# Optimization experiments

Measured on AMD Instinct MI355X. Metric: run time of the kernel, lower is better.

The kernel has to match this reference:

```python
import jax, jax.numpy as jnp
import numpy as np

NUM_HEADS = 16
D_MODEL = 1024
HEAD_DIM = D_MODEL // NUM_HEADS
NEG_BIG = 1e10


def setup_inputs() -> dict:
    key = jax.random.key(0)
    k1, k2, k3 = jax.random.split(key, 3)
    B, T = 2, 2048
    from_tensor = jax.random.normal(k1, (B, T, D_MODEL), dtype=jnp.float32)
    init = 0.02
    Wqkv = jax.random.normal(k2, (D_MODEL, 3 * D_MODEL), dtype=jnp.float32) * init
    bqkv = jnp.zeros((3 * D_MODEL,), dtype=jnp.float32)
    Wproj = jax.random.normal(k3, (D_MODEL, D_MODEL), dtype=jnp.float32) * init
    bproj = jnp.zeros((D_MODEL,), dtype=jnp.float32)
    return {"from_tensor": from_tensor, "Wqkv": Wqkv, "bqkv": bqkv,
            "Wproj": Wproj, "bproj": bproj}


def reference(from_tensor, Wqkv, bqkv, Wproj, bproj):
    B, T, D = from_tensor.shape
    H, hd = NUM_HEADS, D // NUM_HEADS
    qkv = from_tensor @ Wqkv + bqkv                      # [B,T,3D]
    q, k, v = jnp.split(qkv, 3, axis=-1)
    def heads(x):  # [B,T,D] -> [B,H,T,hd]
        return x.reshape(B, T, H, hd).transpose(0, 2, 1, 3)
    q, k, v = heads(q), heads(k), heads(v)
    present = jnp.stack([k, v], axis=1)                  # [B,2,H,T,hd]
    scores = jnp.einsum('bhqd,bhkd->bhqk', q, k)         # [B,H,T,T]
    scores = scores * jax.lax.rsqrt(jnp.float32(hd))
    # faithful mask: m = i > j - ns + nd (strict; diagonal masked)
    nd = ns = T
    i = jnp.arange(nd)[:, None]
    j = jnp.arange(ns)
    m = (i > j - ns + nd).astype(scores.dtype)           # [T,T]
    scores = scores * m - NEG_BIG * (1.0 - m)
    probs = jax.nn.softmax(scores, axis=-1)
    ctx = jnp.einsum('bhqk,bhkd->bhqd', probs, v)        # [B,H,T,hd]
    ctx = ctx.transpose(0, 2, 1, 3).reshape(B, T, D)
    out = ctx @ Wproj + bproj                            # [B,T,D]
    return out, present
```

## Files before the change

### kernel.cpp

```cpp
#include <hip/hip_runtime.h>
#include <hip/hip_bf16.h>
#include <cstdint>

typedef __bf16 bf16_t;
typedef __bf16 bf16x4 __attribute__((ext_vector_type(4)));
typedef __bf16 bf16x8 __attribute__((ext_vector_type(8)));
typedef float  f32x4  __attribute__((ext_vector_type(4)));

#define MFMA16(a,b,c) __builtin_amdgcn_mfma_f32_16x16x32_bf16(a,b,c,0,0,0)

__device__ __forceinline__ void gl_lds16(const void* g, void* l){
    __builtin_amdgcn_global_load_lds(
        (const __attribute__((address_space(1))) void*)g,
        (__attribute__((address_space(3))) void*)l, 16, 0, 0);
}

__global__ void k_cvt(const float* __restrict__ src, bf16_t* __restrict__ dst, int n4){
    int stride = gridDim.x * blockDim.x;
    for (int i = blockIdx.x * blockDim.x + threadIdx.x; i < n4; i += stride){
        float4 v = ((const float4*)src)[i];
        bf16x4 o = { (bf16_t)v.x, (bf16_t)v.y, (bf16_t)v.z, (bf16_t)v.w };
        ((bf16x4*)dst)[i] = o;
    }
}

__global__ void k_transpose_cvt(const float* __restrict__ src, bf16_t* __restrict__ dst,
                                int R, int C){
    __shared__ bf16_t tile[32][33];
    int c0 = blockIdx.x * 32, r0 = blockIdx.y * 32;
    int tx = threadIdx.x & 31, g = threadIdx.x >> 5;
#pragma unroll
    for (int p = 0; p < 4; ++p){
        int r = g + p * 8;
        tile[r][tx] = (bf16_t)src[(size_t)(r0 + r) * C + c0 + tx];
    }
    __syncthreads();
#pragma unroll
    for (int p = 0; p < 4; ++p){
        int rr = g + p * 8;
        dst[(size_t)(c0 + rr) * R + r0 + tx] = tile[tx][rr];
    }
}

template<int MODE>
__global__ void k_gemm(const bf16_t* __restrict__ A, const bf16_t* __restrict__ Bt,
                       const float* __restrict__ bias,
                       float* __restrict__ Cout,
                       bf16_t* __restrict__ qws, bf16_t* __restrict__ kws,
                       bf16_t* __restrict__ vws,
                       int M, int N, int K){
    __shared__ bf16_t sA[128 * 64];
    __shared__ bf16_t sB[128 * 64];
    int m0 = blockIdx.x * 128, n0 = blockIdx.y * 128;
    int tid = threadIdx.x, lane = tid & 63, w = tid >> 6;
    int lr = lane & 15, lg = lane >> 4;
    int wm = (w >> 1) * 64, wn = (w & 1) * 64;
    f32x4 acc[4][4] = {};

    int srow = lane >> 3;
    int scol = ((lane & 7) ^ srow) * 8;

    for (int k0 = 0; k0 < K; k0 += 64){
#pragma unroll
        for (int p = 0; p < 4; ++p){
            int c = w + p * 4;
            gl_lds16(A  + (size_t)(m0 + c * 8 + srow) * K + k0 + scol, &sA[c * 512]);
            gl_lds16(Bt + (size_t)(n0 + c * 8 + srow) * K + k0 + scol, &sB[c * 512]);
        }
        __syncthreads();
#pragma unroll
        for (int ks = 0; ks < 2; ++ks){
            bf16x8 af[4], bfm[4];
            int ca = ((ks * 4 + lg) ^ (lr & 7)) * 8;
#pragma unroll
            for (int i = 0; i < 4; ++i){
                af[i]  = *(const bf16x8*)(sA + (wm + i * 16 + lr) * 64 + ca);
                bfm[i] = *(const bf16x8*)(sB + (wn + i * 16 + lr) * 64 + ca);
            }
#pragma unroll
            for (int i = 0; i < 4; ++i)
#pragma unroll
                for (int j = 0; j < 4; ++j)
                    acc[i][j] = MFMA16(af[i], bfm[j], acc[i][j]);
        }
        __syncthreads();
    }

#pragma unroll
    for (int j = 0; j < 4; ++j){
        int n = n0 + wn + j * 16 + lr;
        float bv = bias[n];
#pragma unroll
        for (int i = 0; i < 4; ++i){
            int mbase = m0 + wm + i * 16 + lg * 4;
#pragma unroll
            for (int r = 0; r < 4; ++r){
                float cv = acc[i][j][r] + bv;
                int m = mbase + r;
                if (MODE == 1){
                    Cout[(size_t)m * N + n] = cv;
                } else {
                    int b = m >> 11, t = m & 2047;
                    int sec = n >> 10, rem = n & 1023;
                    int h = rem >> 6, d = rem & 63;
                    size_t hbase = (((size_t)b * 16 + h) * 2048 + t) * 64;
                    if (sec == 0){
                        qws[hbase + d] = (bf16_t)cv;
                    } else if (sec == 1){
                        kws[hbase + (d ^ ((t & 7) << 3))] = (bf16_t)cv;
                        Cout[((((size_t)b * 2 + 0) * 16 + h) * 2048 + t) * 64 + d] = cv;
                    } else {
                        int tl = t & 63;
                        int sp = (tl & 0x23) | ((tl & 0x0C) << 1) | ((tl & 0x10) >> 2);
                        vws[(((size_t)b * 16 + h) * 64 + d) * 2048 + (t & ~63)
                            + (sp ^ ((d & 7) << 3))] = (bf16_t)cv;
                        Cout[((((size_t)b * 2 + 1) * 16 + h) * 2048 + t) * 64 + d] = cv;
                    }
                }
            }
        }
    }
}

__device__ __forceinline__ void stage_kv8(const bf16_t* khead, const bf16_t* vhead,
                                          bf16_t* sKb, bf16_t* sVb,
                                          int kv0, int w, int lane){
    gl_lds16(khead + (size_t)(kv0 + w * 8 + (lane >> 3)) * 64 + (lane & 7) * 8,
             sKb + w * 512);
    gl_lds16(vhead + (size_t)(w * 8 + (lane >> 3)) * 2048 + kv0 + (lane & 7) * 8,
             sVb + w * 512);
}

__global__ __launch_bounds__(512, 2) void k_flash(const bf16_t* __restrict__ qb,
                        const bf16_t* __restrict__ kb, const bf16_t* __restrict__ vt,
                        bf16_t* __restrict__ ctx){
    __shared__ bf16_t sK[3][4096];
    __shared__ bf16_t sV[3][4096];
    int bid = blockIdx.x;
    int wid = (bid & 7) * 32 + (bid >> 3);
    int bh = wid >> 3;
    int pr = wid & 7;
    int b = bh >> 4, h = bh & 15;
    int tid = threadIdx.x, lane = tid & 63, w = tid >> 6;
    int lr = lane & 15, lg = lane >> 4;
    const bf16_t* qhead = qb + (size_t)bh * 131072;
    const bf16_t* khead = kb + (size_t)bh * 131072;
    const bf16_t* vhead = vt + (size_t)bh * 131072;
    const float SC = 0.18033688f;

    for (int half = 0; half < 2; ++half){
        int qt = half ? 15 - pr : pr;
        int q0 = qt * 128;
        int nkt = 2 * qt + 2;

        bf16x8 aq0, aq1;
        {
            const bf16_t* p = qhead + (size_t)(q0 + w * 16 + lr) * 64 + lg * 8;
            bf16x8 r0 = *(const bf16x8*)p, r1 = *(const bf16x8*)(p + 32);
#pragma unroll
            for (int j = 0; j < 8; ++j){
                aq0[j] = (bf16_t)((float)r0[j] * SC);
                aq1[j] = (bf16_t)((float)r1[j] * SC);
            }
        }
        float m2 = -INFINITY, lsum = 0.f;
        f32x4 oacc[4] = {};

        bf16_t *cK = sK[0], *cV = sV[0];
        bf16_t *nK = sK[1], *nV = sV[1];
        bf16_t *xK = sK[2], *xV = sV[2];
        stage_kv8(khead, vhead, cK, cV, 0, w, lane);
        stage_kv8(khead, vhead, nK, nV, 64, w, lane);

        for (int kt = 0; kt < nkt; ++kt){
            asm volatile("s_waitcnt vmcnt(2)" ::: "memory");
            __builtin_amdgcn_s_barrier();
            {
                int nt = kt + 2; if (nt > nkt - 1) nt = nkt - 1;
                stage_kv8(khead, vhead, xK, xV, nt * 64, w, lane);
            }

            f32x4 s[4];
            __builtin_amdgcn_s_setprio(1);
#pragma unroll
            for (int cf = 0; cf < 4; ++cf){
                f32x4 a = {};
#pragma unroll
                for (int ks = 0; ks < 2; ++ks){
                    bf16x8 ak = *(const bf16x8*)(&cK[(cf * 16 + lr) * 64 + ((ks * 32 + lg * 8) ^ ((lr & 7) << 3))]);
                    a = MFMA16(ak, ks ? aq1 : aq0, a);
                }
                s[cf] = a;
            }
            __builtin_amdgcn_s_setprio(0);
            if (kt >= 2 * qt){
                int qi = q0 + w * 16 + lr;
                int kvg = kt * 64;
#pragma unroll
                for (int cf = 0; cf < 4; ++cf){
                    int kvb = kvg + cf * 16 + lg * 4;
#pragma unroll
                    for (int r = 0; r < 4; ++r)
                        if (qi <= kvb + r) s[cf][r] = -1e10f;
                }
            }
            float pm = s[0][0];
#pragma unroll
            for (int cf = 0; cf < 4; ++cf)
#pragma unroll
                for (int r = 0; r < 4; ++r) pm = fmaxf(pm, s[cf][r]);
            if (!__all(pm - m2 <= 8.f)){
                float pmr = fmaxf(pm, __shfl_xor(pm, 16));
                pmr = fmaxf(pmr, __shfl_xor(pmr, 32));
                float mnew = fmaxf(m2, pmr);
                float alpha = exp2f(m2 - mnew);
                m2 = mnew;
                lsum *= alpha;
                float ar0 = __shfl(alpha, lg * 4 + 0);
                float ar1 = __shfl(alpha, lg * 4 + 1);
                float ar2 = __shfl(alpha, lg * 4 + 2);
                float ar3 = __shfl(alpha, lg * 4 + 3);
#pragma unroll
                for (int df = 0; df < 4; ++df){
                    oacc[df][0] *= ar0; oacc[df][1] *= ar1;
                    oacc[df][2] *= ar2; oacc[df][3] *= ar3;
                }
            }
            float rsum = 0.f;
            bf16x8 ap0, ap1;
#pragma unroll
            for (int cf = 0; cf < 4; ++cf)
#pragma unroll
                for (int r = 0; r < 4; ++r){
                    float pv = exp2f(s[cf][r] - m2);
                    rsum += pv;
                    if (cf < 2) ap0[(cf & 1) * 4 + r] = (bf16_t)pv;
                    else        ap1[(cf & 1) * 4 + r] = (bf16_t)pv;
                }
            lsum += rsum;
            __builtin_amdgcn_s_setprio(1);
#pragma unroll
            for (int ks = 0; ks < 2; ++ks){
                bf16x8 ap = ks ? ap1 : ap0;
#pragma unroll
                for (int df = 0; df < 4; ++df){
                    bf16x8 bv = *(const bf16x8*)(&cV[(df * 16 + lr) * 64 + ((ks * 32 + lg * 8) ^ ((lr & 7) << 3))]);
                    oacc[df] = MFMA16(ap, bv, oacc[df]);
                }
            }
            __builtin_amdgcn_s_setprio(0);
            bf16_t* tK = cK; bf16_t* tV = cV;
            cK = nK; cV = nV; nK = xK; nV = xV; xK = tK; xV = tV;
        }
        asm volatile("s_waitcnt vmcnt(0)" ::: "memory");
        __builtin_amdgcn_s_barrier();

        float lt = lsum;
        lt += __shfl_xor(lt, 16);
        lt += __shfl_xor(lt, 32);
        float ls0 = __shfl(lt, lg * 4 + 0);
        float ls1 = __shfl(lt, lg * 4 + 1);
        float ls2 = __shfl(lt, lg * 4 + 2);
        float ls3 = __shfl(lt, lg * 4 + 3);
#pragma unroll
        for (int df = 0; df < 4; ++df){
            int d = df * 16 + lr;
            int tb = q0 + w * 16 + lg * 4;
            size_t base = ((size_t)b * 2048 + tb) * 1024 + h * 64 + d;
            ctx[base]        = (bf16_t)(oacc[df][0] / ls0);
            ctx[base + 1024] = (bf16_t)(oacc[df][1] / ls1);
            ctx[base + 2048] = (bf16_t)(oacc[df][2] / ls2);
            ctx[base + 3072] = (bf16_t)(oacc[df][3] / ls3);
        }
    }
}

__global__ void k_row0fix(const bf16_t* __restrict__ vt, bf16_t* __restrict__ ctx){
    int bh = blockIdx.y;
    int b = bh >> 4, h = bh & 15;
    int lane = threadIdx.x & 63, w = threadIdx.x >> 6;
    int d = blockIdx.x * 4 + w;
    const bf16_t* row = vt + ((size_t)bh * 64 + d) * 2048;
    float s = 0.f;
#pragma unroll
    for (int k = 0; k < 4; ++k){
        bf16x8 v = *(const bf16x8*)(row + (lane + k * 64) * 8);
#pragma unroll
        for (int j = 0; j < 8; ++j) s += (float)v[j];
    }
#pragma unroll
    for (int off = 1; off < 64; off <<= 1) s += __shfl_xor(s, off);
    if (lane == 0)
        ctx[(size_t)b * 2048 * 1024 + h * 64 + d] = (bf16_t)(s * (1.f / 2048.f));
}

extern "C" void kernel_launch(void* const* d_in, const int* in_sizes, int n_in,
                              void* d_out, int out_size, void* d_ws, size_t ws_size,
                              hipStream_t stream){
    const float* X     = (const float*)d_in[0];
    const float* Wqkv  = (const float*)d_in[1];
    const float* bqkv  = (const float*)d_in[2];
    const float* Wproj = (const float*)d_in[3];
    const float* bproj = (const float*)d_in[4];
    float* out = (float*)d_out;
    float* present = out + 4194304;

    char* ws = (char*)d_ws;
    bf16_t* Xb     = (bf16_t*)(ws);
    bf16_t* WqkvT  = (bf16_t*)(ws + 8388608);
    bf16_t* WprojT = (bf16_t*)(ws + 14680064);
    bf16_t* Qb     = (bf16_t*)(ws + 16777216);
    bf16_t* Kb     = (bf16_t*)(ws + 25165824);
    bf16_t* Vt     = (bf16_t*)(ws + 33554432);
    bf16_t* CTXb   = (bf16_t*)(ws + 41943040);

    k_cvt<<<2048, 256, 0, stream>>>(X, Xb, 4194304 / 4);
    k_transpose_cvt<<<dim3(3072 / 32, 1024 / 32), 256, 0, stream>>>(Wqkv, WqkvT, 1024, 3072);
    k_transpose_cvt<<<dim3(1024 / 32, 1024 / 32), 256, 0, stream>>>(Wproj, WprojT, 1024, 1024);
    k_gemm<0><<<dim3(32, 24), 256, 0, stream>>>(Xb, WqkvT, bqkv, present, Qb, Kb, Vt, 4096, 3072, 1024);
    k_flash<<<256, 512, 0, stream>>>(Qb, Kb, Vt, CTXb);
    k_row0fix<<<dim3(16, 32), 256, 0, stream>>>(Vt, CTXb);
    k_gemm<1><<<dim3(32, 8), 256, 0, stream>>>(CTXb, WprojT, bproj, out, nullptr, nullptr, nullptr, 4096, 1024, 1024);
}
```

Before: 116.0 us.

## Process two query row blocks per wave and drop paired-tile causal balancing

Result: slower. 138.9 us (+19.7%).

```diff
diff --git a/kernel.cpp b/kernel.cpp
--- a/kernel.cpp
+++ b/kernel.cpp
@@ -122,140 +122,155 @@
     }
 }
 
-__device__ __forceinline__ void stage_kv8(const bf16_t* khead, const bf16_t* vhead,
+__device__ __forceinline__ void stage_kv4(const bf16_t* khead, const bf16_t* vhead,
                                           bf16_t* sKb, bf16_t* sVb,
                                           int kv0, int w, int lane){
-    gl_lds16(khead + (size_t)(kv0 + w * 8 + (lane >> 3)) * 64 + (lane & 7) * 8,
-             sKb + w * 512);
-    gl_lds16(vhead + (size_t)(w * 8 + (lane >> 3)) * 2048 + kv0 + (lane & 7) * 8,
-             sVb + w * 512);
-}
-
-__global__ __launch_bounds__(512, 2) void k_flash(const bf16_t* __restrict__ qb,
+#pragma unroll
+    for (int p = 0; p < 2; ++p){
+        int c = w + p * 4;
+        gl_lds16(khead + (size_t)(kv0 + c * 8 + (lane >> 3)) * 64 + (lane & 7) * 8,
+                 sKb + c * 512);
+        gl_lds16(vhead + (size_t)(c * 8 + (lane >> 3)) * 2048 + kv0 + (lane & 7) * 8,
+                 sVb + c * 512);
+    }
+}
+
+__global__ __launch_bounds__(256, 2) void k_flash(const bf16_t* __restrict__ qb,
                         const bf16_t* __restrict__ kb, const bf16_t* __restrict__ vt,
                         bf16_t* __restrict__ ctx){
     __shared__ bf16_t sK[3][4096];
     __shared__ bf16_t sV[3][4096];
     int bid = blockIdx.x;
-    int wid = (bid & 7) * 32 + (bid >> 3);
-    int bh = wid >> 3;
-    int pr = wid & 7;
+    int wid = (bid & 7) * 64 + (bid >> 3);
+    int bh = wid >> 4;
+    int qt = 15 - (wid & 15);
     int b = bh >> 4, h = bh & 15;
     int tid = threadIdx.x, lane = tid & 63, w = tid >> 6;
     int lr = lane & 15, lg = lane >> 4;
+    int q0 = qt * 128;
+    int nkt = 2 * qt + 2;
     const bf16_t* qhead = qb + (size_t)bh * 131072;
     const bf16_t* khead = kb + (size_t)bh * 131072;
     const bf16_t* vhead = vt + (size_t)bh * 131072;
     const float SC = 0.18033688f;
 
-    for (int half = 0; half < 2; ++half){
-        int qt = half ? 15 - pr : pr;
-        int q0 = qt * 128;
-        int nkt = 2 * qt + 2;
-
-        bf16x8 aq0, aq1;
+    bf16x8 aq[2][2];
+#pragma unroll
+    for (int rb = 0; rb < 2; ++rb){
+        const bf16_t* p = qhead + (size_t)(q0 + w * 32 + rb * 16 + lr) * 64 + lg * 8;
+        bf16x8 r0 = *(const bf16x8*)p, r1 = *(const bf16x8*)(p + 32);
+#pragma unroll
+        for (int j = 0; j < 8; ++j){
+            aq[rb][0][j] = (bf16_t)((float)r0[j] * SC);
+            aq[rb][1][j] = (bf16_t)((float)r1[j] * SC);
+        }
+    }
+    float m2[2] = {-INFINITY, -INFINITY};
+    float lsum[2] = {0.f, 0.f};
+    f32x4 oacc[2][4] = {};
+
+    bf16_t *cK = sK[0], *cV = sV[0];
+    bf16_t *nK = sK[1], *nV = sV[1];
+    bf16_t *xK = sK[2], *xV = sV[2];
+    stage_kv4(khead, vhead, cK, cV, 0, w, lane);
+    stage_kv4(khead, vhead, nK, nV, 64, w, lane);
+
+    for (int kt = 0; kt < nkt; ++kt){
+        asm volatile("s_waitcnt vmcnt(4)" ::: "memory");
+        __builtin_amdgcn_s_barrier();
         {
-            const bf16_t* p = qhead + (size_t)(q0 + w * 16 + lr) * 64 + lg * 8;
-            bf16x8 r0 = *(const bf16x8*)p, r1 = *(const bf16x8*)(p + 32);
-#pragma unroll
-            for (int j = 0; j < 8; ++j){
-                aq0[j] = (bf16_t)((float)r0[j] * SC);
-                aq1[j] = (bf16_t)((float)r1[j] * SC);
-            }
-        }
-        float m2 = -INFINITY, lsum = 0.f;
-        f32x4 oacc[4] = {};
-
-        bf16_t *cK = sK[0], *cV = sV[0];
-        bf16_t *nK = sK[1], *nV = sV[1];
-        bf16_t *xK = sK[2], *xV = sV[2];
-        stage_kv8(khead, vhead, cK, cV, 0, w, lane);
-        stage_kv8(khead, vhead, nK, nV, 64, w, lane);
-
-        for (int kt = 0; kt < nkt; ++kt){
-            asm volatile("s_waitcnt vmcnt(2)" ::: "memory");
-            __builtin_amdgcn_s_barrier();
-            {
-                int nt = kt + 2; if (nt > nkt - 1) nt = nkt - 1;
-                stage_kv8(khead, vhead, xK, xV, nt * 64, w, lane);
-            }
-
-            f32x4 s[4];
-            __builtin_amdgcn_s_setprio(1);
-#pragma unroll
-            for (int cf = 0; cf < 4; ++cf){
-                f32x4 a = {};
-#pragma unroll
-                for (int ks = 0; ks < 2; ++ks){
-                    bf16x8 ak = *(const bf16x8*)(&cK[(cf * 16 + lr) * 64 + ((ks * 32 + lg * 8) ^ ((lr & 7) << 3))]);
-                    a = MFMA16(ak, ks ? aq1 : aq0, a);
-                }
-                s[cf] = a;
-            }
-            __builtin_amdgcn_s_setprio(0);
-            if (kt >= 2 * qt){
-                int qi = q0 + w * 16 + lr;
-                int kvg = kt * 64;
+            int nt = kt + 2; if (nt > nkt - 1) nt = nkt - 1;
+            stage_kv4(khead, vhead, xK, xV, nt * 64, w, lane);
+        }
+
+        f32x4 s[2][4];
+        __builtin_amdgcn_s_setprio(1);
+#pragma unroll
+        for (int cf = 0; cf < 4; ++cf){
+            bf16x8 ak0 = *(const bf16x8*)(&cK[(cf * 16 + lr) * 64 + ((lg * 8) ^ ((lr & 7) << 3))]);
+            bf16x8 ak1 = *(const bf16x8*)(&cK[(cf * 16 + lr) * 64 + ((32 + lg * 8) ^ ((lr & 7) << 3))]);
+            f32x4 z = {};
+            s[0][cf] = MFMA16(ak1, aq[0][1], MFMA16(ak0, aq[0][0], z));
+            s[1][cf] = MFMA16(ak1, aq[1][1], MFMA16(ak0, aq[1][0], z));
+        }
+        __builtin_amdgcn_s_setprio(0);
+        if (kt >= 2 * qt){
+            int kvg = kt * 64;
+#pragma unroll
+            for (int rb = 0; rb < 2; ++rb){
+                int qi = q0 + w * 32 + rb * 16 + lr;
 #pragma unroll
                 for (int cf = 0; cf < 4; ++cf){
                     int kvb = kvg + cf * 16 + lg * 4;
 #pragma unroll
                     for (int r = 0; r < 4; ++r)
-                        if (qi <= kvb + r) s[cf][r] = -1e10f;
+                        if (qi <= kvb + r) s[rb][cf][r] = -1e10f;
                 }
             }
-            float pm = s[0][0];
+        }
+        float pm[2];
+#pragma unroll
+        for (int rb = 0; rb < 2; ++rb){
+            float v = s[rb][0][0];
 #pragma unroll
             for (int cf = 0; cf < 4; ++cf)
 #pragma unroll
-                for (int r = 0; r < 4; ++r) pm = fmaxf(pm, s[cf][r]);
-            if (!__all(pm - m2 <= 8.f)){
-                float pmr = fmaxf(pm, __shfl_xor(pm, 16));
+                for (int r = 0; r < 4; ++r) v = fmaxf(v, s[rb][cf][r]);
+            pm[rb] = v;
+        }
+        if (!__all(fmaxf(pm[0] - m2[0], pm[1] - m2[1]) <= 8.f)){
+#pragma unroll
+            for (int rb = 0; rb < 2; ++rb){
+                float pmr = fmaxf(pm[rb], __shfl_xor(pm[rb], 16));
                 pmr = fmaxf(pmr, __shfl_xor(pmr, 32));
-                float mnew = fmaxf(m2, pmr);
-                float alpha = exp2f(m2 - mnew);
-                m2 = mnew;
-                lsum *= alpha;
+                float mnew = fmaxf(m2[rb], pmr);
+                float alpha = exp2f(m2[rb] - mnew);
+                m2[rb] = mnew;
+                lsum[rb] *= alpha;
                 float ar0 = __shfl(alpha, lg * 4 + 0);
                 float ar1 = __shfl(alpha, lg * 4 + 1);
                 float ar2 = __shfl(alpha, lg * 4 + 2);
                 float ar3 = __shfl(alpha, lg * 4 + 3);
 #pragma unroll
                 for (int df = 0; df < 4; ++df){
-                    oacc[df][0] *= ar0; oacc[df][1] *= ar1;
-                    oacc[df][2] *= ar2; oacc[df][3] *= ar3;
+                    oacc[rb][df][0] *= ar0; oacc[rb][df][1] *= ar1;
+                    oacc[rb][df][2] *= ar2; oacc[rb][df][3] *= ar3;
                 }
             }
+        }
+        bf16x8 ap[2][2];
+#pragma unroll
+        for (int rb = 0; rb < 2; ++rb){
             float rsum = 0.f;
-            bf16x8 ap0, ap1;
 #pragma unroll
             for (int cf = 0; cf < 4; ++cf)
 #pragma unroll
                 for (int r = 0; r < 4; ++r){
-                    float pv = exp2f(s[cf][r] - m2);
+                    float pv = exp2f(s[rb][cf][r] - m2[rb]);
                     rsum += pv;
-                    if (cf < 2) ap0[(cf & 1) * 4 + r] = (bf16_t)pv;
-                    else        ap1[(cf & 1) * 4 + r] = (bf16_t)pv;
+                    ap[rb][cf >> 1][(cf & 1) * 4 + r] = (bf16_t)pv;
                 }
-            lsum += rsum;
-            __builtin_amdgcn_s_setprio(1);
-#pragma unroll
-            for (int ks = 0; ks < 2; ++ks){
-                bf16x8 ap = ks ? ap1 : ap0;
-#pragma unroll
-                for (int df = 0; df < 4; ++df){
-                    bf16x8 bv = *(const bf16x8*)(&cV[(df * 16 + lr) * 64 + ((ks * 32 + lg * 8) ^ ((lr & 7) << 3))]);
-                    oacc[df] = MFMA16(ap, bv, oacc[df]);
-                }
-            }
-            __builtin_amdgcn_s_setprio(0);
-            bf16_t* tK = cK; bf16_t* tV = cV;
-            cK = nK; cV = nV; nK = xK; nV = xV; xK = tK; xV = tV;
-        }
-        asm volatile("s_waitcnt vmcnt(0)" ::: "memory");
-        __builtin_amdgcn_s_barrier();
-
-        float lt = lsum;
+            lsum[rb] += rsum;
+        }
+        __builtin_amdgcn_s_setprio(1);
+#pragma unroll
+        for (int ks = 0; ks < 2; ++ks){
+#pragma unroll
+            for (int df = 0; df < 4; ++df){
+                bf16x8 bv = *(const bf16x8*)(&cV[(df * 16 + lr) * 64 + ((ks * 32 + lg * 8) ^ ((lr & 7) << 3))]);
+                oacc[0][df] = MFMA16(ap[0][ks], bv, oacc[0][df]);
+                oacc[1][df] = MFMA16(ap[1][ks], bv, oacc[1][df]);
+            }
+        }
+        __builtin_amdgcn_s_setprio(0);
+        bf16_t* tK = cK; bf16_t* tV = cV;
+        cK = nK; cV = nV; nK = xK; nV = xV; xK = tK; xV = tV;
+    }
+    asm volatile("s_waitcnt vmcnt(0)" ::: "memory");
+
+#pragma unroll
+    for (int rb = 0; rb < 2; ++rb){
+        float lt = lsum[rb];
         lt += __shfl_xor(lt, 16);
         lt += __shfl_xor(lt, 32);
         float ls0 = __shfl(lt, lg * 4 + 0);
@@ -265,12 +280,12 @@
 #pragma unroll
         for (int df = 0; df < 4; ++df){
             int d = df * 16 + lr;
-            int tb = q0 + w * 16 + lg * 4;
+            int tb = q0 + w * 32 + rb * 16 + lg * 4;
             size_t base = ((size_t)b * 2048 + tb) * 1024 + h * 64 + d;
-            ctx[base]        = (bf16_t)(oacc[df][0] / ls0);
-            ctx[base + 1024] = (bf16_t)(oacc[df][1] / ls1);
-            ctx[base + 2048] = (bf16_t)(oacc[df][2] / ls2);
-            ctx[base + 3072] = (bf16_t)(oacc[df][3] / ls3);
+            ctx[base]        = (bf16_t)(oacc[rb][df][0] / ls0);
+            ctx[base + 1024] = (bf16_t)(oacc[rb][df][1] / ls1);
+            ctx[base + 2048] = (bf16_t)(oacc[rb][df][2] / ls2);
+            ctx[base + 3072] = (bf16_t)(oacc[rb][df][3] / ls3);
         }
     }
 }
@@ -318,7 +333,7 @@
     k_transpose_cvt<<<dim3(3072 / 32, 1024 / 32), 256, 0, stream>>>(Wqkv, WqkvT, 1024, 3072);
     k_transpose_cvt<<<dim3(1024 / 32, 1024 / 32), 256, 0, stream>>>(Wproj, WprojT, 1024, 1024);
     k_gemm<0><<<dim3(32, 24), 256, 0, stream>>>(Xb, WqkvT, bqkv, present, Qb, Kb, Vt, 4096, 3072, 1024);
-    k_flash<<<256, 512, 0, stream>>>(Qb, Kb, Vt, CTXb);
+    k_flash<<<512, 256, 0, stream>>>(Qb, Kb, Vt, CTXb);
     k_row0fix<<<dim3(16, 32), 256, 0, stream>>>(Vt, CTXb);
     k_gemm<1><<<dim3(32, 8), 256, 0, stream>>>(CTXb, WprojT, bproj, out, nullptr, nullptr, nullptr, 4096, 1024, 1024);
 }
```
